# Performance work log

Measured on AMD Instinct MI355X. Metric: run time of the kernel, lower is better.

Reference implementation:

```python
import jax, jax.numpy as jnp
import numpy as np

POOL = 7
H, W, C = 200, 200, 512
NUM_ROIS = 128


def setup_inputs() -> dict:
    key = jax.random.key(0)
    k1, k2, k3 = jax.random.split(key, 3)
    img = jax.random.normal(k1, (1, H, W, C), dtype=jnp.float32)
    # (x, y, w, h) in feature-map pixels; w,h >= POOL+1 so every bin is >=1px,
    # and x+w <= W, y+h <= H so crops stay in bounds (as the original assumes).
    wh = jax.random.uniform(k2, (1, NUM_ROIS, 2), minval=float(POOL + 1), maxval=64.0)
    xy = jax.random.uniform(k3, (1, NUM_ROIS, 2)) * (jnp.array([W, H], jnp.float32) - wh)
    rois = jnp.concatenate([xy, wh], axis=-1).astype(jnp.float32)
    return {"img": img, "rois": rois, "pool_size": POOL}


def _roi_pool(x, rois, P):
    # x: (H, W, C) feature map; rois: (R, 4) as (x, y, w, h) floats.
    h_dim, w_dim, _ = x.shape
    ks = jnp.arange(P + 1, dtype=jnp.float32)
    rows = jnp.arange(h_dim)
    cols = jnp.arange(w_dim)

    def pool_one(roi):
        rx, ry, rw, rh = roi[0], roi[1], roi[2], roi[3]
        # Bin boundaries: original computes x1 = int(x + ix*w/P), x2 = int(x + (ix+1)*w/P),
        # i.e. contiguous non-overlapping segments [b[k], b[k+1]).
        bx = (rx + ks * (rw / P)).astype(jnp.int32)
        by = (ry + ks * (rh / P)).astype(jnp.int32)
        # Map each row/col to its bin id; out-of-roi pixels -> dummy segment P.
        rid = jnp.searchsorted(by, rows, side='right') - 1
        rid = jnp.where((rid < 0) | (rid >= P), P, rid)
        cid = jnp.searchsorted(bx, cols, side='right') - 1
        cid = jnp.where((cid < 0) | (cid >= P), P, cid)
        # Max-reduce rows into y-bins, then cols into x-bins (separable rect max).
        rm = jax.ops.segment_max(x, rid, num_segments=P + 1)                     # (P+1, W, C) [jy, w, c]
        cm = jax.ops.segment_max(rm.transpose(1, 0, 2), cid, num_segments=P + 1)  # (P+1, P+1, C) [ix, jy, c]
        return cm[:P, :P].transpose(1, 0, 2)  # (jy, ix, c)

    return jax.vmap(pool_one)(rois)  # (R, P, P, C)


def reference(img, rois, pool_size):
    # Output: (1, num_rois, pool_size, pool_size, channels), tf dim ordering.
    out = _roi_pool(img[0], rois[0], pool_size)
    return out[None]
```

## Files before the change

kernel.cpp:

```cpp
#include <hip/hip_runtime.h>


#define IMG_H 200
#define IMG_W 200
#define IMG_C 512
#define C4 (IMG_C / 4)
#define POOL 7
#define NROI 128
#define PLANES 4

typedef float f4v __attribute__((ext_vector_type(4)));

__device__ __forceinline__ float4 max4(float4 a, float4 b) {
    return make_float4(fmaxf(a.x, b.x), fmaxf(a.y, b.y),
                       fmaxf(a.z, b.z), fmaxf(a.w, b.w));
}

__global__ __launch_bounds__(PLANES * 128, 8) void roi_pool_kernel(
    const float* __restrict__ img,
    const float* __restrict__ rois,
    float* __restrict__ out)
{
    const int bin = blockIdx.x % (POOL * POOL);
    const int roi = blockIdx.x / (POOL * POOL);
    const int jy = bin / POOL;
    const int ix = bin % POOL;

    const float rx = rois[roi * 4 + 0];
    const float ry = rois[roi * 4 + 1];
    const float rw = rois[roi * 4 + 2];
    const float rh = rois[roi * 4 + 3];

    const float sx = __fdiv_rn(rw, 7.0f);
    const float sy = __fdiv_rn(rh, 7.0f);
    const int x1 = (int)__fadd_rn(rx, __fmul_rn((float)ix,       sx));
    const int x2 = (int)__fadd_rn(rx, __fmul_rn((float)(ix + 1), sx));
    const int y1 = (int)__fadd_rn(ry, __fmul_rn((float)jy,       sy));
    const int y2 = (int)__fadd_rn(ry, __fmul_rn((float)(jy + 1), sy));

    const int c4 = threadIdx.x & 127;
    const int p  = threadIdx.x >> 7;
    const float4* __restrict__ img4 = (const float4*)img;

    const int bw = x2 - x1;
    const int bh = y2 - y1;
    const int area = bw * bh;

    const float4 NEG = make_float4(-INFINITY, -INFINITY, -INFINITY, -INFINITY);
    float4 m = NEG;

    int dx = p, dy = 0;
    while (dx >= bw) { dx -= bw; ++dy; }
    #pragma unroll 2
    for (int i = p; i < area; i += PLANES) {
        const size_t px = (size_t)(y1 + dy) * IMG_W + (size_t)(x1 + dx);
        m = max4(m, img4[px * C4 + c4]);
        dx += PLANES;
        while (dx >= bw) { dx -= bw; ++dy; }
    }

    __shared__ float4 red[PLANES - 1][C4];
    if (p > 0) red[p - 1][c4] = m;
    __syncthreads();
    if (p == 0) {
        m = max4(m, red[0][c4]);
        m = max4(m, red[1][c4]);
        m = max4(m, red[2][c4]);

        float4* __restrict__ out4 = (float4*)out;
        f4v* __restrict__ dst =
            (f4v*)&out4[((size_t)(roi * POOL + jy) * POOL + ix) * C4 + c4];
        __builtin_nontemporal_store(*(const f4v*)&m, dst);
    }
}

extern "C" void kernel_launch(void* const* d_in, const int* in_sizes, int n_in,
                              void* d_out, int out_size, void* d_ws, size_t ws_size,
                              hipStream_t stream) {
    (void)in_sizes; (void)n_in; (void)d_ws; (void)ws_size; (void)out_size;
    const float* img  = (const float*)d_in[0];
    const float* rois = (const float*)d_in[1];
    float* out = (float*)d_out;

    dim3 grid(NROI * POOL * POOL);
    dim3 block(PLANES * 128);
    roi_pool_kernel<<<grid, block, 0, stream>>>(img, rois, out);
}
```

Baseline: 140.2 us.

## Assign spatially clustered ROIs to the same XCD via Morton-order ranking

Each block now computes Morton codes of all ROI centers in shared memory and ranks them. Blocks round-robined onto the same XCD (blockIdx mod 8) are then given a contiguous run of 16 spatially nearby ROIs. Overlapping ROIs therefore share the same XCD-local L2, with the aim of raising L2 hit rates on image reads. The cost is redundant per-block ROI loading, an O(N^2) rank loop and two extra barriers. It also depends on the hardware dispatching blocks to XCDs round-robin.

After: 153.1 us. +9.2%, slower.

```diff
diff --git a/kernel.cpp b/kernel.cpp
--- a/kernel.cpp
+++ b/kernel.cpp
@@ -8,6 +8,9 @@
 #define POOL 7
 #define NROI 128
 #define PLANES 4
+#define NXCD 8
+#define NBIN (POOL * POOL)
+#define ROIS_PER_XCD (NROI / NXCD)
 
 typedef float f4v __attribute__((ext_vector_type(4)));
 
@@ -16,13 +19,53 @@
                        fmaxf(a.z, b.z), fmaxf(a.w, b.w));
 }
 
+__device__ __forceinline__ unsigned spread8(unsigned x) {
+    x &= 0xFFu;
+    x = (x | (x << 4)) & 0x0F0Fu;
+    x = (x | (x << 2)) & 0x3333u;
+    x = (x | (x << 1)) & 0x5555u;
+    return x;
+}
+
 __global__ __launch_bounds__(PLANES * 128, 8) void roi_pool_kernel(
     const float* __restrict__ img,
     const float* __restrict__ rois,
     float* __restrict__ out)
 {
-    const int bin = blockIdx.x % (POOL * POOL);
-    const int roi = blockIdx.x / (POOL * POOL);
+    __shared__ unsigned short s_key[NROI];
+    __shared__ int s_roi;
+    __shared__ float4 red[PLANES - 1][C4];
+
+    const int tid = threadIdx.x;
+
+    const int xcd  = blockIdx.x & (NXCD - 1);
+    const int ixcd = blockIdx.x >> 3;
+    const int rank = xcd * ROIS_PER_XCD + ixcd / NBIN;
+    const int bin  = ixcd % NBIN;
+
+    if (tid < NROI) {
+        const float rx = rois[tid * 4 + 0];
+        const float ry = rois[tid * 4 + 1];
+        const float rw = rois[tid * 4 + 2];
+        const float rh = rois[tid * 4 + 3];
+        const unsigned cx = (unsigned)(int)(rx + 0.5f * rw);
+        const unsigned cy = (unsigned)(int)(ry + 0.5f * rh);
+        s_key[tid] = (unsigned short)((spread8(cy) << 1) | spread8(cx));
+    }
+    __syncthreads();
+    if (tid < NROI) {
+        const unsigned my = s_key[tid];
+        int r = 0;
+        #pragma unroll 8
+        for (int u = 0; u < NROI; ++u) {
+            const unsigned ku = s_key[u];
+            r += (int)((ku < my) | ((ku == my) & (u < tid)));
+        }
+        if (r == rank) s_roi = tid;
+    }
+    __syncthreads();
+    const int roi = s_roi;
+
     const int jy = bin / POOL;
     const int ix = bin % POOL;
 
@@ -38,13 +81,14 @@
     const int y1 = (int)__fadd_rn(ry, __fmul_rn((float)jy,       sy));
     const int y2 = (int)__fadd_rn(ry, __fmul_rn((float)(jy + 1), sy));
 
-    const int c4 = threadIdx.x & 127;
-    const int p  = threadIdx.x >> 7;
+    const int c4 = tid & 127;
+    const int p  = tid >> 7;
     const float4* __restrict__ img4 = (const float4*)img;
 
     const int bw = x2 - x1;
     const int bh = y2 - y1;
     const int area = bw * bh;
+    (void)bh;
 
     const float4 NEG = make_float4(-INFINITY, -INFINITY, -INFINITY, -INFINITY);
     float4 m = NEG;
@@ -59,7 +103,6 @@
         while (dx >= bw) { dx -= bw; ++dy; }
     }
 
-    __shared__ float4 red[PLANES - 1][C4];
     if (p > 0) red[p - 1][c4] = m;
     __syncthreads();
     if (p == 0) {
@@ -82,7 +125,7 @@
     const float* rois = (const float*)d_in[1];
     float* out = (float*)d_out;
 
-    dim3 grid(NROI * POOL * POOL);
+    dim3 grid(NROI * NBIN);
     dim3 block(PLANES * 128);
     roi_pool_kernel<<<grid, block, 0, stream>>>(img, rois, out);
 }
```

## Schedule ROI bins across XCDs by spatial locality with a device-built table

Applied to the files above, without the earlier changes.

Adds a small single-block kernel that sorts ROIs by Morton order of their centers, splits them into eight area-balanced chunks, and writes a block-to-work table. Blocks are interleaved so that each XCD (assumed to receive blockIdx round-robin) processes a spatially coherent group of ROIs, which is meant to improve per-XCD L2 reuse of overlapping feature-map pixels. The cost is an extra serial kernel launch with a single-thread prefix loop, plus a table lookup in the main kernel. The table path is used only when workspace is provided, and the XCD-mapping assumption may not hold.

Measured after the change: 187.5 us. 1.34x slower.

```diff
diff --git a/kernel.cpp b/kernel.cpp
--- a/kernel.cpp
+++ b/kernel.cpp
@@ -8,6 +8,10 @@
 #define POOL 7
 #define NROI 128
 #define PLANES 4
+#define NXCD 8
+#define NBIN (POOL * POOL)
+#define NITEM (NROI * NBIN)
+#define SLOTS_PER_XCD (NITEM / NXCD)
 
 typedef float f4v __attribute__((ext_vector_type(4)));
 
@@ -16,13 +20,119 @@
                        fmaxf(a.z, b.z), fmaxf(a.w, b.w));
 }
 
+__device__ __forceinline__ int imin(int a, int b) { return a < b ? a : b; }
+__device__ __forceinline__ int imax(int a, int b) { return a > b ? a : b; }
+
+__device__ __forceinline__ unsigned spread8(unsigned x) {
+    x &= 0xFFu;
+    x = (x | (x << 4)) & 0x0F0Fu;
+    x = (x | (x << 2)) & 0x3333u;
+    x = (x | (x << 1)) & 0x5555u;
+    return x;
+}
+
+__global__ __launch_bounds__(NROI) void build_schedule(
+    const float* __restrict__ rois,
+    unsigned short* __restrict__ table)
+{
+    __shared__ unsigned short key[NROI];
+    __shared__ unsigned char  perm[NROI];
+    __shared__ float          area[NROI];
+    __shared__ float          pref[NROI + 1];
+    __shared__ int            chunk_of[NROI];
+    __shared__ int            rstart[NXCD];
+    __shared__ int            len[NXCD];
+    __shared__ int            spillpre[NXCD + 1];
+    __shared__ int            freepre[NXCD + 1];
+
+    const int t = threadIdx.x;
+
+    const float rx = rois[t * 4 + 0];
+    const float ry = rois[t * 4 + 1];
+    const float rw = rois[t * 4 + 2];
+    const float rh = rois[t * 4 + 3];
+    {
+        const unsigned cx = (unsigned)(int)(rx + 0.5f * rw);
+        const unsigned cy = (unsigned)(int)(ry + 0.5f * rh);
+        key[t] = (unsigned short)((spread8(cy) << 1) | spread8(cx));
+    }
+    __syncthreads();
+
+    {
+        const unsigned my = key[t];
+        int r = 0;
+        #pragma unroll 8
+        for (int u = 0; u < NROI; ++u) {
+            const unsigned ku = key[u];
+            r += (int)((ku < my) | ((ku == my) & (u < t)));
+        }
+        perm[r] = (unsigned char)t;
+        area[r] = rw * rh;
+    }
+    __syncthreads();
+
+    if (t == 0) {
+        float s = 0.f;
+        pref[0] = 0.f;
+        for (int i = 0; i < NROI; ++i) { s += area[i]; pref[i + 1] = s; }
+        const float inv = (float)NXCD / s;
+        int prev = 0;
+        for (int i = 0; i < NROI; ++i) {
+            int c = (int)((pref[i] + 0.5f * area[i]) * inv);
+            c = imin(c, NXCD - 1);
+            c = imax(c, prev);
+            prev = c;
+            chunk_of[i] = c;
+        }
+        for (int x = 0; x < NXCD; ++x) { rstart[x] = 0; len[x] = 0; }
+        for (int i = NROI - 1; i >= 0; --i) rstart[chunk_of[i]] = i;
+        for (int i = 0; i < NROI; ++i) len[chunk_of[i]] += NBIN;
+        int sp = 0, fp = 0;
+        for (int x = 0; x < NXCD; ++x) {
+            spillpre[x] = sp;
+            freepre[x]  = fp;
+            sp += imax(0, len[x] - SLOTS_PER_XCD);
+            fp += imax(0, SLOTS_PER_XCD - len[x]);
+        }
+        spillpre[NXCD] = sp;
+        freepre[NXCD]  = fp;
+    }
+    __syncthreads();
+
+    const int x    = chunk_of[t];
+    const int base = (t - rstart[x]) * NBIN;
+    const int roi  = (int)perm[t];
+    for (int m = 0; m < NBIN; ++m) {
+        const int j = base + m;
+        const unsigned short e = (unsigned short)((roi << 6) | m);
+        if (j < SLOTS_PER_XCD) {
+            table[j * NXCD + x] = e;
+        } else {
+            const int si = spillpre[x] + (j - SLOTS_PER_XCD);
+            int y = 0;
+            while (!(si >= freepre[y] && si < freepre[y + 1])) ++y;
+            const int fy = freepre[y + 1] - freepre[y];
+            const int k  = (SLOTS_PER_XCD - fy) + (si - freepre[y]);
+            table[k * NXCD + y] = e;
+        }
+    }
+}
+
 __global__ __launch_bounds__(PLANES * 128, 8) void roi_pool_kernel(
     const float* __restrict__ img,
     const float* __restrict__ rois,
+    const unsigned short* __restrict__ table,
     float* __restrict__ out)
 {
-    const int bin = blockIdx.x % (POOL * POOL);
-    const int roi = blockIdx.x / (POOL * POOL);
+    int roi, bin;
+    if (table) {
+        const unsigned e = (unsigned)table[blockIdx.x];
+        roi = (int)(e >> 6);
+        bin = (int)(e & 63u);
+    } else {
+        roi = blockIdx.x / NBIN;
+        bin = blockIdx.x % NBIN;
+    }
     const int jy = bin / POOL;
     const int ix = bin % POOL;
 
@@ -43,8 +153,7 @@
     const float4* __restrict__ img4 = (const float4*)img;
 
     const int bw = x2 - x1;
-    const int bh = y2 - y1;
-    const int area = bw * bh;
+    const int area = bw * (y2 - y1);
 
     const float4 NEG = make_float4(-INFINITY, -INFINITY, -INFINITY, -INFINITY);
     float4 m = NEG;
@@ -77,12 +186,18 @@
 extern "C" void kernel_launch(void* const* d_in, const int* in_sizes, int n_in,
                               void* d_out, int out_size, void* d_ws, size_t ws_size,
                               hipStream_t stream) {
-    (void)in_sizes; (void)n_in; (void)d_ws; (void)ws_size; (void)out_size;
+    (void)in_sizes; (void)n_in; (void)out_size;
     const float* img  = (const float*)d_in[0];
     const float* rois = (const float*)d_in[1];
     float* out = (float*)d_out;
 
-    dim3 grid(NROI * POOL * POOL);
-    dim3 block(PLANES * 128);
-    roi_pool_kernel<<<grid, block, 0, stream>>>(img, rois, out);
-}
+    const bool use_table =
+        (d_ws != nullptr) && (ws_size >= NITEM * sizeof(unsigned short));
+    unsigned short* table = use_table ? (unsigned short*)d_ws : nullptr;
+
+    if (use_table)
+        build_schedule<<<dim3(1), dim3(NROI), 0, stream>>>(rois, table);
+
+    roi_pool_kernel<<<dim3(NITEM), dim3(PLANES * 128), 0, stream>>>(
+        img, rois, table, out);
+}
```

## Remap blocks to XCDs by Morton-sorted ROI locality with area balancing

Applied to the files above, without the earlier changes.

Each block now sorts all ROIs by the Morton code of their center inside one wavefront, prefix-sums ROI areas, and splits the sorted ROIs into eight area-balanced groups. Overflow work is spilled into slots left free by other groups, and blockIdx is mapped so that blocks landing on the same XCD (round-robin by blockIdx mod 8) handle spatially nearby ROIs. The goal is to improve per-XCD L2 reuse of image pixels shared by overlapping ROIs and to balance load across XCDs. The cost is a redundant 64-lane sort and scan in every block plus an extra barrier before the main loop.

Result: slower. 160.8 us (+14.7%).

```diff
diff --git a/kernel.cpp b/kernel.cpp
--- a/kernel.cpp
+++ b/kernel.cpp
@@ -8,12 +8,27 @@
 #define POOL 7
 #define NROI 128
 #define PLANES 4
+#define NXCD 8
+#define NBIN (POOL * POOL)
+#define NITEM (NROI * NBIN)
+#define SLOTS_PER_XCD (NITEM / NXCD)
 
 typedef float f4v __attribute__((ext_vector_type(4)));
 
 __device__ __forceinline__ float4 max4(float4 a, float4 b) {
     return make_float4(fmaxf(a.x, b.x), fmaxf(a.y, b.y),
                        fmaxf(a.z, b.z), fmaxf(a.w, b.w));
+}
+
+__device__ __forceinline__ int imin(int a, int b) { return a < b ? a : b; }
+__device__ __forceinline__ int imax(int a, int b) { return a > b ? a : b; }
+
+__device__ __forceinline__ unsigned spread8(unsigned x) {
+    x &= 0xFFu;
+    x = (x | (x << 4)) & 0x0F0Fu;
+    x = (x | (x << 2)) & 0x3333u;
+    x = (x | (x << 1)) & 0x5555u;
+    return x;
 }
 
 __global__ __launch_bounds__(PLANES * 128, 8) void roi_pool_kernel(
@@ -21,8 +36,118 @@
     const float* __restrict__ rois,
     float* __restrict__ out)
 {
-    const int bin = blockIdx.x % (POOL * POOL);
-    const int roi = blockIdx.x / (POOL * POOL);
+    __shared__ int    s_perm[NROI];
+    __shared__ float  s_area[NROI];
+    __shared__ int    s_len[NXCD];
+    __shared__ int    s_rstart[NXCD];
+    __shared__ int    s_spillpre[NXCD + 1];
+    __shared__ int    s_freepre[NXCD + 1];
+    __shared__ int    s_roi, s_bin;
+    __shared__ float4 red[PLANES - 1][C4];
+
+    const int tid = threadIdx.x;
+
+    if (tid < 64) {
+        const int lane = tid;
+        const float4* __restrict__ rois4 = (const float4*)rois;
+        const float4 ra = rois4[lane];
+        const float4 rb = rois4[lane + 64];
+
+        const unsigned cxa = (unsigned)(int)(ra.x + 0.5f * ra.z);
+        const unsigned cya = (unsigned)(int)(ra.y + 0.5f * ra.w);
+        const unsigned cxb = (unsigned)(int)(rb.x + 0.5f * rb.z);
+        const unsigned cyb = (unsigned)(int)(rb.y + 0.5f * rb.w);
+        const int keyA = (int)((spread8(cya) << 1) | spread8(cxa));
+        const int keyB = (int)((spread8(cyb) << 1) | spread8(cxb));
+
+        int rankA = 0, rankB = 0;
+        for (int d = 0; d < 64; ++d) {
+            const int oA = __shfl(keyA, d);
+            const int oB = __shfl(keyB, d);
+            rankA += (int)((oA < keyA) | ((oA == keyA) & (d < lane)));
+            rankA += (int)(oB < keyA);
+            rankB += (int)(oA <= keyB);
+            rankB += (int)((oB < keyB) | ((oB == keyB) & (d < lane)));
+        }
+        s_perm[rankA] = lane;
+        s_perm[rankB] = lane + 64;
+        s_area[rankA] = ra.z * ra.w;
+        s_area[rankB] = rb.z * rb.w;
+        __threadfence_block();
+
+        const float aLo = s_area[lane];
+        const float aHi = s_area[lane + 64];
+        float pLo = aLo;
+        #pragma unroll
+        for (int d = 1; d < 64; d <<= 1) {
+            const float o = __shfl_up(pLo, d);
+            if (lane >= d) pLo += o;
+        }
+        const float totLo = __shfl(pLo, 63);
+        float pHi = aHi;
+        #pragma unroll
+        for (int d = 1; d < 64; d <<= 1) {
+            const float o = __shfl_up(pHi, d);
+            if (lane >= d) pHi += o;
+        }
+        pHi += totLo;
+        const float total = __shfl(pHi, 63);
+
+        const float scale = (float)NXCD / total;
+        const int cLo = imin((int)((pLo - 0.5f * aLo) * scale), NXCD - 1);
+        const int cHi = imin((int)((pHi - 0.5f * aHi) * scale), NXCD - 1);
+
+        int myCnt = 0, myPre = 0;
+        #pragma unroll
+        for (int c = 0; c < NXCD; ++c) {
+            const int n = __popcll(__ballot(cLo == c)) +
+                          __popcll(__ballot(cHi == c));
+            if (lane == c) myCnt = n;
+            if (lane >  c) myPre += n;
+        }
+        const int myLen = myCnt * NBIN;
+        int ov = imax(myLen - SLOTS_PER_XCD, 0);
+        int fr = imax(SLOTS_PER_XCD - myLen, 0);
+        int ovI = ov, frI = fr;
+        #pragma unroll
+        for (int d = 1; d < 8; d <<= 1) {
+            const int o = __shfl_up(ovI, d);
+            const int f = __shfl_up(frI, d);
+            if (lane >= d) { ovI += o; frI += f; }
+        }
+        if (lane < NXCD) {
+            s_len[lane]      = myLen;
+            s_rstart[lane]   = myPre;
+            s_spillpre[lane] = ovI - ov;
+            s_freepre[lane]  = frI - fr;
+        }
+        if (lane == NXCD - 1) { s_spillpre[NXCD] = ovI; s_freepre[NXCD] = frI; }
+        __threadfence_block();
+
+        if (lane == 0) {
+            const int x = blockIdx.x & (NXCD - 1);
+            const int j = blockIdx.x >> 3;
+            int tt, mm;
+            const int lenx = s_len[x];
+            if (j < lenx) {
+                tt = s_rstart[x] + j / NBIN;
+                mm = j % NBIN;
+            } else {
+                const int si = s_freepre[x] + (j - lenx);
+                int xx = 0;
+                while (!(si >= s_spillpre[xx] && si < s_spillpre[xx + 1])) ++xx;
+                const int jj = SLOTS_PER_XCD + (si - s_spillpre[xx]);
+                tt = s_rstart[xx] + jj / NBIN;
+                mm = jj % NBIN;
+            }
+            s_roi = s_perm[tt];
+            s_bin = mm;
+        }
+    }
+    __syncthreads();
+
+    const int roi = s_roi;
+    const int bin = s_bin;
     const int jy = bin / POOL;
     const int ix = bin % POOL;
 
@@ -38,13 +163,12 @@
     const int y1 = (int)__fadd_rn(ry, __fmul_rn((float)jy,       sy));
     const int y2 = (int)__fadd_rn(ry, __fmul_rn((float)(jy + 1), sy));
 
-    const int c4 = threadIdx.x & 127;
-    const int p  = threadIdx.x >> 7;
+    const int c4 = tid & 127;
+    const int p  = tid >> 7;
     const float4* __restrict__ img4 = (const float4*)img;
 
     const int bw = x2 - x1;
-    const int bh = y2 - y1;
-    const int area = bw * bh;
+    const int area = bw * (y2 - y1);
 
     const float4 NEG = make_float4(-INFINITY, -INFINITY, -INFINITY, -INFINITY);
     float4 m = NEG;
@@ -59,7 +183,6 @@
         while (dx >= bw) { dx -= bw; ++dy; }
     }
 
-    __shared__ float4 red[PLANES - 1][C4];
     if (p > 0) red[p - 1][c4] = m;
     __syncthreads();
     if (p == 0) {
@@ -82,7 +205,6 @@
     const float* rois = (const float*)d_in[1];
     float* out = (float*)d_out;
 
-    dim3 grid(NROI * POOL * POOL);
-    dim3 block(PLANES * 128);
-    roi_pool_kernel<<<grid, block, 0, stream>>>(img, rois, out);
-}
+    roi_pool_kernel<<<dim3(NITEM), dim3(PLANES * 128), 0, stream>>>(
+        img, rois, out);
+}
```
